# Optimization experiments

Measured on AMD Instinct MI355X. Metric: run time of the kernel, lower is better.

## Reference

```python
import jax, jax.numpy as jnp
import numpy as np

N_NODES = 50000
N_EDGES = 600000
D = 128        # input_dim == hidden_dim
OUT = 2        # output_dim
N_LAYERS = 6


def setup_inputs() -> dict:
    key = jax.random.key(0)
    ks = jax.random.split(key, 6)
    scale = 1.0 / np.sqrt(D)
    x = jax.random.normal(ks[0], (N_NODES, D), jnp.float32)
    edge_index = jax.random.randint(ks[1], (2, N_EDGES), 0, N_NODES)
    Wl = jax.random.normal(ks[2], (N_LAYERS, D, D), jnp.float32) * scale  # neighbor (lin_l) weights
    Wr = jax.random.normal(ks[3], (N_LAYERS, D, D), jnp.float32) * scale  # root (lin_r) weights
    bl = jnp.zeros((N_LAYERS, D), jnp.float32)                            # lin_l bias
    fc_W = jax.random.normal(ks[4], (D, OUT), jnp.float32) * scale
    fc_b = jnp.zeros((OUT,), jnp.float32)
    return {"x": x, "edge_index": edge_index, "Wl": Wl, "Wr": Wr, "bl": bl,
            "fc_W": fc_W, "fc_b": fc_b}


def _sage_conv(h, src, dst, deg_inv, Wl_i, Wr_i, bl_i):
    # mean aggregation over incoming edges: gather -> scatter-add -> normalize
    agg = jax.ops.segment_sum(h[src], dst, num_segments=h.shape[0]) * deg_inv  # [N, D]
    return agg @ Wl_i + h @ Wr_i + bl_i


def reference(x, edge_index, Wl, Wr, bl, fc_W, fc_b):
    src, dst = edge_index[0], edge_index[1]
    deg = jax.ops.segment_sum(jnp.ones(src.shape, x.dtype), dst, num_segments=x.shape[0])
    deg_inv = (1.0 / jnp.maximum(deg, 1.0))[:, None]  # [N, 1]
    h = x
    # ReLU follows every SAGEConv: inner act of each GraphSAGE block + explicit F.relu after each block
    for i in range(N_LAYERS):
        h = _sage_conv(h, src, dst, deg_inv, Wl[i], Wr[i], bl[i])
        h = jax.nn.relu(h)
    return h @ fc_W + fc_b  # [N, OUT]
```

## Files before the change

kernel.cpp:

```cpp
#include <hip/hip_runtime.h>
#include <hip/hip_bf16.h>

#define N_NODES 50000
#define N_EDGES 600000
#define DD 128
#define N_LAYERS 6
#define SCAN_BLOCKS 196
#define N_CHUNKS 3125
#define AGG_BLOCKS 6256

#define XB16_T 1600000
#define PREPW_T 196608
#define PREP_TOTAL (XB16_T + PREPW_T + N_EDGES)

typedef __attribute__((ext_vector_type(8))) short bf16x8;
typedef __attribute__((ext_vector_type(4))) float floatx4;

__device__ __forceinline__ unsigned short f2b(float f) {
    unsigned u = __float_as_uint(f);
    unsigned r = (u + 0x7FFFu + ((u >> 16) & 1u)) >> 16;
    return (unsigned short)r;
}


__global__ void prep_all(const float* __restrict__ x, unsigned short* __restrict__ hx,
                         const float* __restrict__ Wl, const float* __restrict__ Wr,
                         unsigned short* __restrict__ WT2,
                         const int* __restrict__ dst, int* __restrict__ deg) {
    int gid = blockIdx.x * blockDim.x + threadIdx.x;
    if (gid < XB16_T) {
        int b = gid * 4;
        float4 v = *(const float4*)(x + b);
        ushort4 o;
        o.x = f2b(v.x); o.y = f2b(v.y); o.z = f2b(v.z); o.w = f2b(v.w);
        *(ushort4*)(hx + b) = o;
    } else if (gid < XB16_T + PREPW_T) {
        int idx = gid - XB16_T;
        int l   = idx >> 15;
        int rem = idx & 32767;
        int n   = rem >> 8;
        int k2  = rem & 255;
        const float* W = (k2 < 128 ? Wl : Wr) + (size_t)l * DD * DD + (size_t)(k2 & 127) * DD + n;
        WT2[idx] = f2b(*W);
    } else if (gid < PREP_TOTAL) {
        int e = gid - (XB16_T + PREPW_T);
        atomicAdd(&deg[dst[e]], 1);
    }
}


__global__ void block_sums(const int* __restrict__ deg, int* __restrict__ bsum) {
    __shared__ int s[256];
    int tid = threadIdx.x;
    int i = blockIdx.x * 256 + tid;
    int v = (i < N_NODES) ? deg[i] : 0;
    s[tid] = v;
    __syncthreads();
    #pragma unroll
    for (int off = 128; off > 0; off >>= 1) {
        if (tid < off) s[tid] += s[tid + off];
        __syncthreads();
    }
    if (tid == 0) bsum[blockIdx.x] = s[0];
}

__global__ void scan_bsums(int* __restrict__ bsum, int* __restrict__ offsets) {
    __shared__ int s[256];
    int tid = threadIdx.x;
    int v = (tid < SCAN_BLOCKS) ? bsum[tid] : 0;
    s[tid] = v;
    __syncthreads();
    for (int off = 1; off < 256; off <<= 1) {
        int t = (tid >= off) ? s[tid - off] : 0;
        __syncthreads();
        s[tid] += t;
        __syncthreads();
    }
    if (tid < SCAN_BLOCKS) bsum[tid] = s[tid] - v;
    if (tid == 0) offsets[N_NODES] = N_EDGES;
}

__global__ void write_offsets(const int* __restrict__ deg, const int* __restrict__ bsum,
                              int* __restrict__ offsets, float* __restrict__ deg_inv) {
    __shared__ int s[256];
    int tid = threadIdx.x;
    int i = blockIdx.x * 256 + tid;
    int v = (i < N_NODES) ? deg[i] : 0;
    s[tid] = v;
    __syncthreads();
    for (int off = 1; off < 256; off <<= 1) {
        int t = (tid >= off) ? s[tid - off] : 0;
        __syncthreads();
        s[tid] += t;
        __syncthreads();
    }
    if (i < N_NODES) {
        offsets[i] = bsum[blockIdx.x] + s[tid] - v;
        deg_inv[i] = 1.0f / (float)(v > 1 ? v : 1);
    }
}

__global__ void fill_csr(const int* __restrict__ src, const int* __restrict__ dst,
                         const int* __restrict__ offsets, int* __restrict__ cursor,
                         int* __restrict__ csr_src) {
    int e = blockIdx.x * blockDim.x + threadIdx.x;
    if (e < N_EDGES) {
        int d = dst[e];
        int p = atomicAdd(&cursor[d], 1);
        csr_src[offsets[d] + p] = src[e];
    }
}


__device__ __forceinline__ void acc16(float* a, const uint4& va, const uint4& vb) {
    a[0] += __uint_as_float(va.x << 16); a[1] += __uint_as_float(va.x & 0xFFFF0000u);
    a[2] += __uint_as_float(va.y << 16); a[3] += __uint_as_float(va.y & 0xFFFF0000u);
    a[4] += __uint_as_float(va.z << 16); a[5] += __uint_as_float(va.z & 0xFFFF0000u);
    a[6] += __uint_as_float(va.w << 16); a[7] += __uint_as_float(va.w & 0xFFFF0000u);
    a[8] += __uint_as_float(vb.x << 16); a[9] += __uint_as_float(vb.x & 0xFFFF0000u);
    a[10]+= __uint_as_float(vb.y << 16); a[11]+= __uint_as_float(vb.y & 0xFFFF0000u);
    a[12]+= __uint_as_float(vb.z << 16); a[13]+= __uint_as_float(vb.z & 0xFFFF0000u);
    a[14]+= __uint_as_float(vb.w << 16); a[15]+= __uint_as_float(vb.w & 0xFFFF0000u);
}

__launch_bounds__(256, 8)
__global__ void aggregate(const unsigned short* __restrict__ hin, const int* __restrict__ offsets,
                          const int* __restrict__ csr_src, const float* __restrict__ deg_inv,
                          unsigned short* __restrict__ agg) {
    int w    = threadIdx.x >> 6;
    int lane = threadIdx.x & 63;
    int nodeSel = lane >> 5;
    int l32  = lane & 31;
    int grp  = l32 >> 3;
    int p    = l32 & 7;

    int b = blockIdx.x;
    int x = b & 7, s = b >> 3;
    int hc = 16 * (s >> 1) + 2 * x + (s & 1);
    int node = hc * 8 + 2 * w + nodeSel;
    if (node >= N_NODES) return;
    int s0 = offsets[node], e0 = offsets[node + 1];
    float di = deg_inv[node];

    float a[16];
    #pragma unroll
    for (int i = 0; i < 16; ++i) a[i] = 0.f;

    const unsigned short* base = hin;
    int j = s0 + grp;
    for (; j + 8 < e0; j += 12) {
        int src1 = csr_src[j];
        int src2 = csr_src[j + 4];
        int src3 = csr_src[j + 8];
        const uint4* r1 = (const uint4*)(base + (size_t)src1 * DD + p * 16);
        const uint4* r2 = (const uint4*)(base + (size_t)src2 * DD + p * 16);
        const uint4* r3 = (const uint4*)(base + (size_t)src3 * DD + p * 16);
        uint4 v1a = r1[0], v1b = r1[1];
        uint4 v2a = r2[0], v2b = r2[1];
        uint4 v3a = r3[0], v3b = r3[1];
        acc16(a, v1a, v1b);
        acc16(a, v2a, v2b);
        acc16(a, v3a, v3b);
    }
    if (j + 4 < e0) {
        int src1 = csr_src[j];
        int src2 = csr_src[j + 4];
        const uint4* r1 = (const uint4*)(base + (size_t)src1 * DD + p * 16);
        const uint4* r2 = (const uint4*)(base + (size_t)src2 * DD + p * 16);
        uint4 v1a = r1[0], v1b = r1[1];
        uint4 v2a = r2[0], v2b = r2[1];
        acc16(a, v1a, v1b);
        acc16(a, v2a, v2b);
        j += 8;
    }
    if (j < e0) {
        int src1 = csr_src[j];
        const uint4* r1 = (const uint4*)(base + (size_t)src1 * DD + p * 16);
        uint4 v1a = r1[0], v1b = r1[1];
        acc16(a, v1a, v1b);
    }

    #pragma unroll
    for (int i = 0; i < 16; ++i) {
        a[i] += __shfl_xor(a[i], 8, 64);
        a[i] += __shfl_xor(a[i], 16, 64);
    }

    if (grp == 0) {
        uint4 o1, o2;
        o1.x = (unsigned)f2b(a[0] * di) | ((unsigned)f2b(a[1] * di) << 16);
        o1.y = (unsigned)f2b(a[2] * di) | ((unsigned)f2b(a[3] * di) << 16);
        o1.z = (unsigned)f2b(a[4] * di) | ((unsigned)f2b(a[5] * di) << 16);
        o1.w = (unsigned)f2b(a[6] * di) | ((unsigned)f2b(a[7] * di) << 16);
        o2.x = (unsigned)f2b(a[8] * di) | ((unsigned)f2b(a[9] * di) << 16);
        o2.y = (unsigned)f2b(a[10]* di) | ((unsigned)f2b(a[11]* di) << 16);
        o2.z = (unsigned)f2b(a[12]* di) | ((unsigned)f2b(a[13]* di) << 16);
        o2.w = (unsigned)f2b(a[14]* di) | ((unsigned)f2b(a[15]* di) << 16);
        uint4* dst = (uint4*)(agg + (size_t)node * DD + p * 16);
        dst[0] = o1;
        dst[1] = o2;
    }
}


__launch_bounds__(512, 4)
__global__ void gemm_resW(const unsigned short* __restrict__ Agg,
                          const unsigned short* __restrict__ H,
                          const unsigned short* __restrict__ WT2,
                          const float* __restrict__ bias,
                          unsigned short* __restrict__ Cout,
                          const float* __restrict__ fcW,
                          const float* __restrict__ fcb,
                          float* __restrict__ out,
                          int doFC) {
    __shared__ __align__(16) unsigned short sW[128 * 256];

    int tid  = threadIdx.x;
    int wid  = tid >> 6, lane = tid & 63;
    int l15  = lane & 15, q = lane >> 4;

    for (int t = tid; t < 4096; t += 512) {
        int col = t >> 5, c = t & 31;
        uint4 v = *(const uint4*)(WT2 + (size_t)col * 256 + c * 8);
        *(uint4*)(sW + ((size_t)col * 32 + (c ^ (col & 7))) * 8) = v;
    }
    __syncthreads();

    int chunk = blockIdx.x * 8 + wid;
    if (chunk >= N_CHUNKS) return;
    int row0 = chunk * 16;

    float bcol[8];
    #pragma unroll
    for (int j = 0; j < 8; ++j) bcol[j] = bias[j * 16 + l15];

    const unsigned short* Arow = Agg + (size_t)(row0 + l15) * DD;
    const unsigned short* Hrow = H   + (size_t)(row0 + l15) * DD;
    bf16x8 aF[8];
    #pragma unroll
    for (int s = 0; s < 4; ++s)
        aF[s] = *(const bf16x8*)(Arow + (s * 4 + q) * 8);
    #pragma unroll
    for (int s = 4; s < 8; ++s)
        aF[s] = *(const bf16x8*)(Hrow + (s * 4 + q - 16) * 8);

    floatx4 acc[8];
    #pragma unroll
    for (int j = 0; j < 8; ++j) acc[j] = (floatx4){0.f, 0.f, 0.f, 0.f};

    #pragma unroll
    for (int s = 0; s < 8; ++s) {
        int cglob = s * 4 + q;
        #pragma unroll
        for (int j = 0; j < 8; ++j) {
            int col = j * 16 + l15;
            bf16x8 bF = *(const bf16x8*)(sW + ((size_t)col * 32 + (cglob ^ (col & 7))) * 8);
            acc[j] = __builtin_amdgcn_mfma_f32_16x16x32_bf16(aF[s], bF, acc[j], 0, 0, 0);
        }
    }

    if (!doFC) {
        #pragma unroll
        for (int r = 0; r < 4; ++r) {
            int row = row0 + q * 4 + r;
            #pragma unroll
            for (int j = 0; j < 8; ++j) {
                float v = acc[j][r] + bcol[j];
                Cout[(size_t)row * DD + j * 16 + l15] = f2b(fmaxf(v, 0.f));
            }
        }
    } else {
        float2 fcw[8];
        #pragma unroll
        for (int j = 0; j < 8; ++j) fcw[j] = *(const float2*)(fcW + (j * 16 + l15) * 2);
        float fb0 = fcb[0], fb1 = fcb[1];
        #pragma unroll
        for (int r = 0; r < 4; ++r) {
            float p0 = 0.f, p1 = 0.f;
            #pragma unroll
            for (int j = 0; j < 8; ++j) {
                float v = fmaxf(acc[j][r] + bcol[j], 0.f);
                p0 += v * fcw[j].x;
                p1 += v * fcw[j].y;
            }
            p0 += __shfl_xor(p0, 1, 64); p1 += __shfl_xor(p1, 1, 64);
            p0 += __shfl_xor(p0, 2, 64); p1 += __shfl_xor(p1, 2, 64);
            p0 += __shfl_xor(p0, 4, 64); p1 += __shfl_xor(p1, 4, 64);
            p0 += __shfl_xor(p0, 8, 64); p1 += __shfl_xor(p1, 8, 64);
            if (l15 == 0) {
                int row = row0 + q * 4 + r;
                out[row * 2]     = p0 + fb0;
                out[row * 2 + 1] = p1 + fb1;
            }
        }
    }
}


extern "C" void kernel_launch(void* const* d_in, const int* in_sizes, int n_in,
                              void* d_out, int out_size, void* d_ws, size_t ws_size,
                              hipStream_t stream) {
    const float* x    = (const float*)d_in[0];
    const int*   ei   = (const int*)d_in[1];
    const float* Wl   = (const float*)d_in[2];
    const float* Wr   = (const float*)d_in[3];
    const float* bl   = (const float*)d_in[4];
    const float* fcW  = (const float*)d_in[5];
    const float* fcb  = (const float*)d_in[6];
    float* out = (float*)d_out;

    const int* srcIdx = ei;
    const int* dstIdx = ei + N_EDGES;

    char* ws = (char*)d_ws;
    size_t off = 0;
    auto bump = [&](size_t bytes) { char* p = ws + off; off = (off + bytes + 255) & ~(size_t)255; return p; };
    int*   deg     = (int*)  bump(N_NODES * 4);
    int*   cursor  = (int*)  bump(N_NODES * 4);
    int*   offsets = (int*)  bump((N_NODES + 1) * 4);
    int*   bsum    = (int*)  bump(SCAN_BLOCKS * 4);
    float* deg_inv = (float*)bump(N_NODES * 4);
    int*   csr     = (int*)  bump(N_EDGES * 4);
    unsigned short* hx   = (unsigned short*)bump((size_t)N_NODES * DD * 2);
    unsigned short* hb0  = (unsigned short*)bump((size_t)N_NODES * DD * 2);
    unsigned short* hb1  = (unsigned short*)bump((size_t)N_NODES * DD * 2);
    unsigned short* agg  = (unsigned short*)bump((size_t)N_NODES * DD * 2);
    unsigned short* WT2  = (unsigned short*)bump((size_t)N_LAYERS * 128 * 256 * 2);
    (void)ws_size;

    size_t zbytes = (size_t)((char*)cursor - (char*)deg) + (size_t)N_NODES * 4;
    (void)hipMemsetAsync(deg, 0, zbytes, stream);

    prep_all<<<(PREP_TOTAL + 255) / 256, 256, 0, stream>>>(x, hx, Wl, Wr, WT2, dstIdx, deg);
    block_sums<<<SCAN_BLOCKS, 256, 0, stream>>>(deg, bsum);
    scan_bsums<<<1, 256, 0, stream>>>(bsum, offsets);
    write_offsets<<<SCAN_BLOCKS, 256, 0, stream>>>(deg, bsum, offsets, deg_inv);
    fill_csr<<<(N_EDGES + 255) / 256, 256, 0, stream>>>(srcIdx, dstIdx, offsets, cursor, csr);

    const unsigned short* hin = hx;
    unsigned short* hbuf[2] = { hb0, hb1 };
    for (int l = 0; l < N_LAYERS; ++l) {
        int last = (l == N_LAYERS - 1);
        aggregate<<<AGG_BLOCKS, 256, 0, stream>>>(hin, offsets, csr, deg_inv, agg);
        unsigned short* hout = hbuf[l & 1];
        gemm_resW<<<(N_CHUNKS + 7) / 8, 512, 0, stream>>>(
            agg, hin, WT2 + (size_t)l * 128 * 256, bl + (size_t)l * DD, hout,
            fcW, fcb, out, last);
        hin = hout;
    }
}
```

Measured before the change: 347.0 us.

## Sort nodes by degree for aggregation and merge CSR scan into one kernel

Replaces the three-kernel degree scan with a single 1024-thread block that computes the offsets and also builds a node permutation bucketed by descending degree. The aggregate kernel now walks nodes in that order, so wavefronts handle nodes of similar degree, which is meant to cut load imbalance and divergence inside each wave. It also adds nontemporal loads and stores for x, the CSR indices and the agg output. The cost is a serial single-block scan, scattered per-node writes through the permutation, and the loss of the previous block swizzle, which may have given better locality.

```diff
diff --git a/kernel.cpp b/kernel.cpp
--- a/kernel.cpp
+++ b/kernel.cpp
@@ -5,9 +5,8 @@
 #define N_EDGES 600000
 #define DD 128
 #define N_LAYERS 6
-#define SCAN_BLOCKS 196
 #define N_CHUNKS 3125
-#define AGG_BLOCKS 6256
+#define AGG_BLOCKS 6250
 
 #define XB16_T 1600000
 #define PREPW_T 196608
@@ -15,6 +14,7 @@
 
 typedef __attribute__((ext_vector_type(8))) short bf16x8;
 typedef __attribute__((ext_vector_type(4))) float floatx4;
+typedef __attribute__((ext_vector_type(4))) unsigned int uintx4;
 
 __device__ __forceinline__ unsigned short f2b(float f) {
     unsigned u = __float_as_uint(f);
@@ -30,7 +30,7 @@
     int gid = blockIdx.x * blockDim.x + threadIdx.x;
     if (gid < XB16_T) {
         int b = gid * 4;
-        float4 v = *(const float4*)(x + b);
+        floatx4 v = __builtin_nontemporal_load((const floatx4*)(x + b));
         ushort4 o;
         o.x = f2b(v.x); o.y = f2b(v.y); o.z = f2b(v.z); o.w = f2b(v.w);
         *(ushort4*)(hx + b) = o;
@@ -49,54 +49,59 @@
 }
 
 
-__global__ void block_sums(const int* __restrict__ deg, int* __restrict__ bsum) {
-    __shared__ int s[256];
+#define SCAN_T 1024
+#define SCAN_STRIDE 49
+
+__global__ __launch_bounds__(1024) void csr_scan(const int* __restrict__ deg,
+                                                 int* __restrict__ offsets,
+                                                 float* __restrict__ deg_inv,
+                                                 int* __restrict__ perm) {
+    __shared__ int part[SCAN_T];
+    __shared__ int hist[64];
+    __shared__ int histOff[64];
+
     int tid = threadIdx.x;
-    int i = blockIdx.x * 256 + tid;
-    int v = (i < N_NODES) ? deg[i] : 0;
-    s[tid] = v;
+    if (tid < 64) hist[tid] = 0;
+    int lo = tid * SCAN_STRIDE;
+    int hi = lo + SCAN_STRIDE; if (hi > N_NODES) hi = N_NODES;
     __syncthreads();
-    #pragma unroll
-    for (int off = 128; off > 0; off >>= 1) {
-        if (tid < off) s[tid] += s[tid + off];
+
+    int s = 0;
+    for (int i = lo; i < hi; ++i) {
+        int d = deg[i];
+        s += d;
+        int b = d < 63 ? d : 63;
+        atomicAdd(&hist[b], 1);
+    }
+    part[tid] = s;
+    __syncthreads();
+
+    for (int off = 1; off < SCAN_T; off <<= 1) {
+        int t = (tid >= off) ? part[tid - off] : 0;
         __syncthreads();
-    }
-    if (tid == 0) bsum[blockIdx.x] = s[0];
-}
-
-__global__ void scan_bsums(int* __restrict__ bsum, int* __restrict__ offsets) {
-    __shared__ int s[256];
-    int tid = threadIdx.x;
-    int v = (tid < SCAN_BLOCKS) ? bsum[tid] : 0;
-    s[tid] = v;
+        part[tid] += t;
+        __syncthreads();
+    }
+    int run = part[tid] - s;
+
+    for (int i = lo; i < hi; ++i) {
+        int d = deg[i];
+        offsets[i] = run;
+        run += d;
+        deg_inv[i] = 1.0f / (float)(d > 1 ? d : 1);
+    }
+    if (tid == 0) {
+        offsets[N_NODES] = N_EDGES;
+        int acc = 0;
+        for (int b = 63; b >= 0; --b) { histOff[b] = acc; acc += hist[b]; }
+    }
     __syncthreads();
-    for (int off = 1; off < 256; off <<= 1) {
-        int t = (tid >= off) ? s[tid - off] : 0;
-        __syncthreads();
-        s[tid] += t;
-        __syncthreads();
-    }
-    if (tid < SCAN_BLOCKS) bsum[tid] = s[tid] - v;
-    if (tid == 0) offsets[N_NODES] = N_EDGES;
-}
-
-__global__ void write_offsets(const int* __restrict__ deg, const int* __restrict__ bsum,
-                              int* __restrict__ offsets, float* __restrict__ deg_inv) {
-    __shared__ int s[256];
-    int tid = threadIdx.x;
-    int i = blockIdx.x * 256 + tid;
-    int v = (i < N_NODES) ? deg[i] : 0;
-    s[tid] = v;
-    __syncthreads();
-    for (int off = 1; off < 256; off <<= 1) {
-        int t = (tid >= off) ? s[tid - off] : 0;
-        __syncthreads();
-        s[tid] += t;
-        __syncthreads();
-    }
-    if (i < N_NODES) {
-        offsets[i] = bsum[blockIdx.x] + s[tid] - v;
-        deg_inv[i] = 1.0f / (float)(v > 1 ? v : 1);
+
+    for (int i = lo; i < hi; ++i) {
+        int d = deg[i];
+        int b = d < 63 ? d : 63;
+        int pos = atomicAdd(&histOff[b], 1);
+        perm[pos] = i;
     }
 }
 
@@ -126,6 +131,7 @@
 __launch_bounds__(256, 8)
 __global__ void aggregate(const unsigned short* __restrict__ hin, const int* __restrict__ offsets,
                           const int* __restrict__ csr_src, const float* __restrict__ deg_inv,
+                          const int* __restrict__ perm,
                           unsigned short* __restrict__ agg) {
     int w    = threadIdx.x >> 6;
     int lane = threadIdx.x & 63;
@@ -134,11 +140,8 @@
     int grp  = l32 >> 3;
     int p    = l32 & 7;
 
-    int b = blockIdx.x;
-    int x = b & 7, s = b >> 3;
-    int hc = 16 * (s >> 1) + 2 * x + (s & 1);
-    int node = hc * 8 + 2 * w + nodeSel;
-    if (node >= N_NODES) return;
+    int nodeL = blockIdx.x * 8 + 2 * w + nodeSel;
+    int node = perm[nodeL];
     int s0 = offsets[node], e0 = offsets[node + 1];
     float di = deg_inv[node];
 
@@ -149,9 +152,9 @@
     const unsigned short* base = hin;
     int j = s0 + grp;
     for (; j + 8 < e0; j += 12) {
-        int src1 = csr_src[j];
-        int src2 = csr_src[j + 4];
-        int src3 = csr_src[j + 8];
+        int src1 = __builtin_nontemporal_load(csr_src + j);
+        int src2 = __builtin_nontemporal_load(csr_src + j + 4);
+        int src3 = __builtin_nontemporal_load(csr_src + j + 8);
         const uint4* r1 = (const uint4*)(base + (size_t)src1 * DD + p * 16);
         const uint4* r2 = (const uint4*)(base + (size_t)src2 * DD + p * 16);
         const uint4* r3 = (const uint4*)(base + (size_t)src3 * DD + p * 16);
@@ -163,8 +166,8 @@
         acc16(a, v3a, v3b);
     }
     if (j + 4 < e0) {
-        int src1 = csr_src[j];
-        int src2 = csr_src[j + 4];
+        int src1 = __builtin_nontemporal_load(csr_src + j);
+        int src2 = __builtin_nontemporal_load(csr_src + j + 4);
         const uint4* r1 = (const uint4*)(base + (size_t)src1 * DD + p * 16);
         const uint4* r2 = (const uint4*)(base + (size_t)src2 * DD + p * 16);
         uint4 v1a = r1[0], v1b = r1[1];
@@ -174,7 +177,7 @@
         j += 8;
     }
     if (j < e0) {
-        int src1 = csr_src[j];
+        int src1 = __builtin_nontemporal_load(csr_src + j);
         const uint4* r1 = (const uint4*)(base + (size_t)src1 * DD + p * 16);
         uint4 v1a = r1[0], v1b = r1[1];
         acc16(a, v1a, v1b);
@@ -187,7 +190,7 @@
     }
 
     if (grp == 0) {
-        uint4 o1, o2;
+        uintx4 o1, o2;
         o1.x = (unsigned)f2b(a[0] * di) | ((unsigned)f2b(a[1] * di) << 16);
         o1.y = (unsigned)f2b(a[2] * di) | ((unsigned)f2b(a[3] * di) << 16);
         o1.z = (unsigned)f2b(a[4] * di) | ((unsigned)f2b(a[5] * di) << 16);
@@ -196,9 +199,9 @@
         o2.y = (unsigned)f2b(a[10]* di) | ((unsigned)f2b(a[11]* di) << 16);
         o2.z = (unsigned)f2b(a[12]* di) | ((unsigned)f2b(a[13]* di) << 16);
         o2.w = (unsigned)f2b(a[14]* di) | ((unsigned)f2b(a[15]* di) << 16);
-        uint4* dst = (uint4*)(agg + (size_t)node * DD + p * 16);
-        dst[0] = o1;
-        dst[1] = o2;
+        uintx4* dst = (uintx4*)(agg + (size_t)node * DD + p * 16);
+        __builtin_nontemporal_store(o1, dst);
+        __builtin_nontemporal_store(o2, dst + 1);
     }
 }
 
@@ -318,7 +321,7 @@
     int*   deg     = (int*)  bump(N_NODES * 4);
     int*   cursor  = (int*)  bump(N_NODES * 4);
     int*   offsets = (int*)  bump((N_NODES + 1) * 4);
-    int*   bsum    = (int*)  bump(SCAN_BLOCKS * 4);
+    int*   perm    = (int*)  bump(N_NODES * 4);
     float* deg_inv = (float*)bump(N_NODES * 4);
     int*   csr     = (int*)  bump(N_EDGES * 4);
     unsigned short* hx   = (unsigned short*)bump((size_t)N_NODES * DD * 2);
@@ -332,16 +335,14 @@
     (void)hipMemsetAsync(deg, 0, zbytes, stream);
 
     prep_all<<<(PREP_TOTAL + 255) / 256, 256, 0, stream>>>(x, hx, Wl, Wr, WT2, dstIdx, deg);
-    block_sums<<<SCAN_BLOCKS, 256, 0, stream>>>(deg, bsum);
-    scan_bsums<<<1, 256, 0, stream>>>(bsum, offsets);
-    write_offsets<<<SCAN_BLOCKS, 256, 0, stream>>>(deg, bsum, offsets, deg_inv);
+    csr_scan<<<1, 1024, 0, stream>>>(deg, offsets, deg_inv, perm);
     fill_csr<<<(N_EDGES + 255) / 256, 256, 0, stream>>>(srcIdx, dstIdx, offsets, cursor, csr);
 
     const unsigned short* hin = hx;
     unsigned short* hbuf[2] = { hb0, hb1 };
     for (int l = 0; l < N_LAYERS; ++l) {
         int last = (l == N_LAYERS - 1);
-        aggregate<<<AGG_BLOCKS, 256, 0, stream>>>(hin, offsets, csr, deg_inv, agg);
+        aggregate<<<AGG_BLOCKS, 256, 0, stream>>>(hin, offsets, csr, deg_inv, perm, agg);
         unsigned short* hout = hbuf[l & 1];
         gemm_resW<<<(N_CHUNKS + 7) / 8, 512, 0, stream>>>(
             agg, hin, WT2 + (size_t)l * 128 * 256, bl + (size_t)l * DD, hout,
```

After: 674.1 us. +94.3%, slower.

## Sort nodes by in-degree for load-balanced aggregation and add nontemporal hints

Applied to the files above, without the earlier changes.

Builds a degree histogram and a degree-sorted node permutation (descending) during CSR construction. The aggregate kernel then processes nodes in that order, so wavefronts pair nodes with similar edge counts and suffer less divergence and imbalance. It also adds nontemporal loads and stores for x, the CSR indices and the aggregate output to reduce cache pollution. The cost is extra atomics and a permutation indirection, and it gives up the previous XCD-aware block-to-node mapping, which may lower L2 locality.

```diff
diff --git a/kernel.cpp b/kernel.cpp
--- a/kernel.cpp
+++ b/kernel.cpp
@@ -7,7 +7,7 @@
 #define N_LAYERS 6
 #define SCAN_BLOCKS 196
 #define N_CHUNKS 3125
-#define AGG_BLOCKS 6256
+#define AGG_BLOCKS 6250
 
 #define XB16_T 1600000
 #define PREPW_T 196608
@@ -15,6 +15,7 @@
 
 typedef __attribute__((ext_vector_type(8))) short bf16x8;
 typedef __attribute__((ext_vector_type(4))) float floatx4;
+typedef __attribute__((ext_vector_type(4))) unsigned int uintx4;
 
 __device__ __forceinline__ unsigned short f2b(float f) {
     unsigned u = __float_as_uint(f);
@@ -30,7 +31,7 @@
     int gid = blockIdx.x * blockDim.x + threadIdx.x;
     if (gid < XB16_T) {
         int b = gid * 4;
-        float4 v = *(const float4*)(x + b);
+        floatx4 v = __builtin_nontemporal_load((const floatx4*)(x + b));
         ushort4 o;
         o.x = f2b(v.x); o.y = f2b(v.y); o.z = f2b(v.z); o.w = f2b(v.w);
         *(ushort4*)(hx + b) = o;
@@ -49,45 +50,62 @@
 }
 
 
-__global__ void block_sums(const int* __restrict__ deg, int* __restrict__ bsum) {
+__global__ void block_sums(const int* __restrict__ deg, int* __restrict__ bsum,
+                           int* __restrict__ ghist) {
+    __shared__ int s[256];
+    __shared__ int h[64];
+    int tid = threadIdx.x;
+    if (tid < 64) h[tid] = 0;
+    int i = blockIdx.x * 256 + tid;
+    int v = (i < N_NODES) ? deg[i] : 0;
+    s[tid] = v;
+    __syncthreads();
+    if (i < N_NODES) {
+        int b = v < 63 ? v : 63;
+        atomicAdd(&h[b], 1);
+    }
+    #pragma unroll
+    for (int off = 128; off > 0; off >>= 1) {
+        if (tid < off) s[tid] += s[tid + off];
+        __syncthreads();
+    }
+    if (tid == 0) bsum[blockIdx.x] = s[0];
+    if (tid < 64 && h[tid] > 0) atomicAdd(&ghist[tid], h[tid]);
+}
+
+__global__ void scan_bsums(int* __restrict__ bsum, int* __restrict__ offsets,
+                           const int* __restrict__ ghist, int* __restrict__ binOff) {
+    __shared__ int s[256];
+    __shared__ int hoff[64];
+    int tid = threadIdx.x;
+    int v = (tid < SCAN_BLOCKS) ? bsum[tid] : 0;
+    s[tid] = v;
+    __syncthreads();
+    for (int off = 1; off < 256; off <<= 1) {
+        int t = (tid >= off) ? s[tid - off] : 0;
+        __syncthreads();
+        s[tid] += t;
+        __syncthreads();
+    }
+    if (tid < SCAN_BLOCKS) bsum[tid] = s[tid] - v;
+    if (tid == 0) {
+        offsets[N_NODES] = N_EDGES;
+        int acc = 0;
+        for (int b = 63; b >= 0; --b) { hoff[b] = acc; acc += ghist[b]; }
+    }
+    __syncthreads();
+    if (tid < 64) binOff[tid] = hoff[tid];
+}
+
+__global__ void write_offsets(const int* __restrict__ deg, const int* __restrict__ bsum,
+                              int* __restrict__ offsets, float* __restrict__ deg_inv,
+                              int* __restrict__ binOff, int* __restrict__ perm) {
     __shared__ int s[256];
     int tid = threadIdx.x;
     int i = blockIdx.x * 256 + tid;
     int v = (i < N_NODES) ? deg[i] : 0;
     s[tid] = v;
     __syncthreads();
-    #pragma unroll
-    for (int off = 128; off > 0; off >>= 1) {
-        if (tid < off) s[tid] += s[tid + off];
-        __syncthreads();
-    }
-    if (tid == 0) bsum[blockIdx.x] = s[0];
-}
-
-__global__ void scan_bsums(int* __restrict__ bsum, int* __restrict__ offsets) {
-    __shared__ int s[256];
-    int tid = threadIdx.x;
-    int v = (tid < SCAN_BLOCKS) ? bsum[tid] : 0;
-    s[tid] = v;
-    __syncthreads();
-    for (int off = 1; off < 256; off <<= 1) {
-        int t = (tid >= off) ? s[tid - off] : 0;
-        __syncthreads();
-        s[tid] += t;
-        __syncthreads();
-    }
-    if (tid < SCAN_BLOCKS) bsum[tid] = s[tid] - v;
-    if (tid == 0) offsets[N_NODES] = N_EDGES;
-}
-
-__global__ void write_offsets(const int* __restrict__ deg, const int* __restrict__ bsum,
-                              int* __restrict__ offsets, float* __restrict__ deg_inv) {
-    __shared__ int s[256];
-    int tid = threadIdx.x;
-    int i = blockIdx.x * 256 + tid;
-    int v = (i < N_NODES) ? deg[i] : 0;
-    s[tid] = v;
-    __syncthreads();
     for (int off = 1; off < 256; off <<= 1) {
         int t = (tid >= off) ? s[tid - off] : 0;
         __syncthreads();
@@ -97,6 +115,9 @@
     if (i < N_NODES) {
         offsets[i] = bsum[blockIdx.x] + s[tid] - v;
         deg_inv[i] = 1.0f / (float)(v > 1 ? v : 1);
+        int b = v < 63 ? v : 63;
+        int pos = atomicAdd(&binOff[b], 1);
+        perm[pos] = i;
     }
 }
 
@@ -126,6 +147,7 @@
 __launch_bounds__(256, 8)
 __global__ void aggregate(const unsigned short* __restrict__ hin, const int* __restrict__ offsets,
                           const int* __restrict__ csr_src, const float* __restrict__ deg_inv,
+                          const int* __restrict__ perm,
                           unsigned short* __restrict__ agg) {
     int w    = threadIdx.x >> 6;
     int lane = threadIdx.x & 63;
@@ -134,11 +156,8 @@
     int grp  = l32 >> 3;
     int p    = l32 & 7;
 
-    int b = blockIdx.x;
-    int x = b & 7, s = b >> 3;
-    int hc = 16 * (s >> 1) + 2 * x + (s & 1);
-    int node = hc * 8 + 2 * w + nodeSel;
-    if (node >= N_NODES) return;
+    int nodeL = blockIdx.x * 8 + 2 * w + nodeSel;
+    int node = perm[nodeL];
     int s0 = offsets[node], e0 = offsets[node + 1];
     float di = deg_inv[node];
 
@@ -149,9 +168,9 @@
     const unsigned short* base = hin;
     int j = s0 + grp;
     for (; j + 8 < e0; j += 12) {
-        int src1 = csr_src[j];
-        int src2 = csr_src[j + 4];
-        int src3 = csr_src[j + 8];
+        int src1 = __builtin_nontemporal_load(csr_src + j);
+        int src2 = __builtin_nontemporal_load(csr_src + j + 4);
+        int src3 = __builtin_nontemporal_load(csr_src + j + 8);
         const uint4* r1 = (const uint4*)(base + (size_t)src1 * DD + p * 16);
         const uint4* r2 = (const uint4*)(base + (size_t)src2 * DD + p * 16);
         const uint4* r3 = (const uint4*)(base + (size_t)src3 * DD + p * 16);
@@ -163,8 +182,8 @@
         acc16(a, v3a, v3b);
     }
     if (j + 4 < e0) {
-        int src1 = csr_src[j];
-        int src2 = csr_src[j + 4];
+        int src1 = __builtin_nontemporal_load(csr_src + j);
+        int src2 = __builtin_nontemporal_load(csr_src + j + 4);
         const uint4* r1 = (const uint4*)(base + (size_t)src1 * DD + p * 16);
         const uint4* r2 = (const uint4*)(base + (size_t)src2 * DD + p * 16);
         uint4 v1a = r1[0], v1b = r1[1];
@@ -174,7 +193,7 @@
         j += 8;
     }
     if (j < e0) {
-        int src1 = csr_src[j];
+        int src1 = __builtin_nontemporal_load(csr_src + j);
         const uint4* r1 = (const uint4*)(base + (size_t)src1 * DD + p * 16);
         uint4 v1a = r1[0], v1b = r1[1];
         acc16(a, v1a, v1b);
@@ -187,7 +206,7 @@
     }
 
     if (grp == 0) {
-        uint4 o1, o2;
+        uintx4 o1, o2;
         o1.x = (unsigned)f2b(a[0] * di) | ((unsigned)f2b(a[1] * di) << 16);
         o1.y = (unsigned)f2b(a[2] * di) | ((unsigned)f2b(a[3] * di) << 16);
         o1.z = (unsigned)f2b(a[4] * di) | ((unsigned)f2b(a[5] * di) << 16);
@@ -196,9 +215,9 @@
         o2.y = (unsigned)f2b(a[10]* di) | ((unsigned)f2b(a[11]* di) << 16);
         o2.z = (unsigned)f2b(a[12]* di) | ((unsigned)f2b(a[13]* di) << 16);
         o2.w = (unsigned)f2b(a[14]* di) | ((unsigned)f2b(a[15]* di) << 16);
-        uint4* dst = (uint4*)(agg + (size_t)node * DD + p * 16);
-        dst[0] = o1;
-        dst[1] = o2;
+        uintx4* dst = (uintx4*)(agg + (size_t)node * DD + p * 16);
+        __builtin_nontemporal_store(o1, dst);
+        __builtin_nontemporal_store(o2, dst + 1);
     }
 }
 
@@ -317,8 +336,11 @@
     auto bump = [&](size_t bytes) { char* p = ws + off; off = (off + bytes + 255) & ~(size_t)255; return p; };
     int*   deg     = (int*)  bump(N_NODES * 4);
     int*   cursor  = (int*)  bump(N_NODES * 4);
+    int*   ghist   = (int*)  bump(64 * 4);
+    int*   binOff  = (int*)  bump(64 * 4);
     int*   offsets = (int*)  bump((N_NODES + 1) * 4);
     int*   bsum    = (int*)  bump(SCAN_BLOCKS * 4);
+    int*   perm    = (int*)  bump(N_NODES * 4);
     float* deg_inv = (float*)bump(N_NODES * 4);
     int*   csr     = (int*)  bump(N_EDGES * 4);
     unsigned short* hx   = (unsigned short*)bump((size_t)N_NODES * DD * 2);
@@ -328,20 +350,20 @@
     unsigned short* WT2  = (unsigned short*)bump((size_t)N_LAYERS * 128 * 256 * 2);
     (void)ws_size;
 
-    size_t zbytes = (size_t)((char*)cursor - (char*)deg) + (size_t)N_NODES * 4;
+    size_t zbytes = (size_t)((char*)ghist - (char*)deg) + 64 * 4;
     (void)hipMemsetAsync(deg, 0, zbytes, stream);
 
     prep_all<<<(PREP_TOTAL + 255) / 256, 256, 0, stream>>>(x, hx, Wl, Wr, WT2, dstIdx, deg);
-    block_sums<<<SCAN_BLOCKS, 256, 0, stream>>>(deg, bsum);
-    scan_bsums<<<1, 256, 0, stream>>>(bsum, offsets);
-    write_offsets<<<SCAN_BLOCKS, 256, 0, stream>>>(deg, bsum, offsets, deg_inv);
+    block_sums<<<SCAN_BLOCKS, 256, 0, stream>>>(deg, bsum, ghist);
+    scan_bsums<<<1, 256, 0, stream>>>(bsum, offsets, ghist, binOff);
+    write_offsets<<<SCAN_BLOCKS, 256, 0, stream>>>(deg, bsum, offsets, deg_inv, binOff, perm);
     fill_csr<<<(N_EDGES + 255) / 256, 256, 0, stream>>>(srcIdx, dstIdx, offsets, cursor, csr);
 
     const unsigned short* hin = hx;
     unsigned short* hbuf[2] = { hb0, hb1 };
     for (int l = 0; l < N_LAYERS; ++l) {
         int last = (l == N_LAYERS - 1);
-        aggregate<<<AGG_BLOCKS, 256, 0, stream>>>(hin, offsets, csr, deg_inv, agg);
+        aggregate<<<AGG_BLOCKS, 256, 0, stream>>>(hin, offsets, csr, deg_inv, perm, agg);
         unsigned short* hout = hbuf[l & 1];
         gemm_resW<<<(N_CHUNKS + 7) / 8, 512, 0, stream>>>(
             agg, hin, WT2 + (size_t)l * 128 * 256, bl + (size_t)l * DD, hout,
```

Measured after the change: 677.0 us. 1.95x slower.
